# Performance work log

Hardware: AMD Instinct MI355X
Metric: run time of the kernel (lower is better)

Reference implementation:

```python
import jax, jax.numpy as jnp
import numpy as np

S, B, NINP, NHID, NLAYERS = 512, 128, 128, 128, 3


def setup_inputs() -> dict:
    key = jax.random.key(0)
    ks = jax.random.split(key, 6)
    stdv = 1.0 / float(np.sqrt(NHID))
    u = lambda k, shape: jax.random.uniform(k, shape, jnp.float32, -stdv, stdv)
    return {
        "x": jax.random.normal(ks[0], (S, B, NINP), jnp.float32),
        "lin_w": u(ks[1], (NHID, NINP)),
        "lin_b": u(ks[2], (NHID,)),
        "W": u(ks[3], (NLAYERS, 4 * NHID, NHID)),
        "U": u(ks[4], (NLAYERS, 4 * NHID, NLAYERS * NHID)),
        "G": u(ks[5], (NLAYERS, NHID, 1)),
    }


def reference(x, lin_w, lin_b, W, U, G):
    # x: [S, B, ninp]; eval mode (no dropout masks), feedback=True, gated=True.
    S_, B_, _ = x.shape
    L = W.shape[0]
    H = W.shape[1] // 4
    xp = x @ lin_w.T + lin_b  # [S, B, H] input projection
    h0 = jnp.zeros((L, B_, H), x.dtype)
    c0 = jnp.zeros((L, B_, H), x.dtype)

    def step(carry, xt):
        h, c = carry  # each [L, B, H]
        # gated: per-layer scalar sigmoid gate, broadcast over H
        gh = jax.nn.sigmoid(jnp.einsum('lbh,lho->lbo', h, G))  # [L, B, 1]
        h = gh * h
        # feedback: concat all layers' hidden along features, shared by every layer
        hx = h.transpose(1, 0, 2).reshape(B_, L * H)  # [B, L*H]
        inp = xt  # [B, H]; stacked layers: output of layer i feeds layer i+1
        hs, cs = [], []
        for i in range(L):
            gates = inp @ W[i].T + hx @ U[i].T  # [B, 4H]
            ig, fg, gg, og = jnp.split(gates, 4, axis=-1)
            ig = jax.nn.sigmoid(ig)
            fg = jax.nn.sigmoid(fg)
            gg = jnp.tanh(gg)
            og = jax.nn.sigmoid(og)
            cy = fg * c[i] + ig * gg
            hy = og * jnp.tanh(cy)
            hs.append(hy)
            cs.append(cy)
            inp = hy
        return (jnp.stack(hs, 0), jnp.stack(cs, 0)), None

    (h, c), _ = jax.lax.scan(step, (h0, c0), xp)
    return (h, c)
```

## Files before the change

### kernel.cpp

```cpp
#include <hip/hip_runtime.h>

#define S_LEN 512
#define BATCH 128
#define NH    128
#define NL    3

#define HXS  392
#define INPS 136

#define XP_OFF   0u
#define WP_OFF   16777216u
#define UP_OFF   (WP_OFF + 393216u)
#define HX_OFF   (UP_OFF + 1179648u)
#define HX_SZ    393216u

typedef float f32x4 __attribute__((ext_vector_type(4)));
typedef short bf16x8 __attribute__((ext_vector_type(8)));
typedef unsigned u32x4 __attribute__((ext_vector_type(4)));
typedef unsigned long long u64;

__device__ __forceinline__ short f2bf(float f) {
    unsigned u = __builtin_bit_cast(unsigned, f);
    u = (u + 0x7FFFu + ((u >> 16) & 1u)) >> 16;
    return (short)u;
}
__device__ __forceinline__ float bf2f_lo(unsigned u) { return __builtin_bit_cast(float, u << 16); }
__device__ __forceinline__ float bf2f_hi(unsigned u) { return __builtin_bit_cast(float, u & 0xFFFF0000u); }
__device__ __forceinline__ float chf(const u32x4& q, int r) {
    unsigned wd = (r < 2) ? q[0] : q[1];
    return (r & 1) ? bf2f_hi(wd) : bf2f_lo(wd);
}
__device__ __forceinline__ float sigm(float x) { return 1.f / (1.f + __expf(-x)); }
__device__ __forceinline__ float tanh_fast(float x) { return 2.f / (1.f + __expf(-2.f * x)) - 1.f; }

__global__ __launch_bounds__(128) void xp_kernel(const float* __restrict__ x,
        const float* __restrict__ lin_w, const float* __restrict__ lin_b,
        short* __restrict__ xp) {
    __shared__ float xs[8 * 128];
    const int tid = threadIdx.x;
    const long r0 = (long)blockIdx.x * 8;
    for (int rr = 0; rr < 8; ++rr)
        xs[rr * 128 + tid] = x[(r0 + rr) * 128 + tid];
    __syncthreads();
    float acc[8];
    float bias = lin_b[tid];
    #pragma unroll
    for (int rr = 0; rr < 8; ++rr) acc[rr] = bias;
    const float* wrow = lin_w + (long)tid * 128;
    for (int k = 0; k < 128; ++k) {
        float wv = wrow[k];
        #pragma unroll
        for (int rr = 0; rr < 8; ++rr) acc[rr] += xs[rr * 128 + k] * wv;
    }
    for (int rr = 0; rr < 8; ++rr)
        xp[(r0 + rr) * 128 + tid] = f2bf(acc[rr]);
}

__global__ __launch_bounds__(256) void pack_kernel(const float* __restrict__ W,
        const float* __restrict__ U, short* __restrict__ Wp, short* __restrict__ Up) {
    int id = blockIdx.x * 256 + threadIdx.x;
    int lane = id & 63;
    int fid = id >> 6;
    int n = lane & 15, lk = lane >> 4;
    if (fid < 384) {
        int kt = fid & 3, w = (fid >> 2) & 3, unit = fid >> 4;
        int l = unit >> 3, c = unit & 7;
        int row = (n >> 2) * 128 + c * 16 + w * 4 + (n & 3);
        const float* src = W + ((long)(l * 512 + row)) * 128 + kt * 32 + lk * 8;
        short* dst = Wp + (long)fid * 512 + lane * 8;
        #pragma unroll
        for (int j = 0; j < 8; ++j) dst[j] = f2bf(src[j]);
    } else {
        int f = fid - 384;
        int kt = f % 12, gu = f / 12;
        int w = gu & 3, unit = gu >> 2;
        int l = unit >> 3, c = unit & 7;
        int row = (n >> 2) * 128 + c * 16 + w * 4 + (n & 3);
        const float* src = U + ((long)(l * 512 + row)) * 384 + kt * 32 + lk * 8;
        short* dst = Up + (long)f * 512 + lane * 8;
        #pragma unroll
        for (int j = 0; j < 8; ++j) dst[j] = f2bf(src[j]);
    }
}


__global__ __launch_bounds__(256, 1) void lstm_kernel(
    const short* __restrict__ xp, const short* __restrict__ Wp,
    const short* __restrict__ Up, const float* __restrict__ Gp,
    char* __restrict__ hexch, float* __restrict__ out)
{
    __shared__ short hx_lds[16 * HXS];
    __shared__ short inp_lds[16 * INPS];
    __shared__ float G_lds[NL * 128];
    __shared__ unsigned hxflag;

    const int tid  = threadIdx.x;
    const int lane = tid & 63;
    const int w    = tid >> 6;
    const int lr   = lane & 15;
    const int lk   = lane >> 4;
    const int grp  = blockIdx.x & 7;
    const int unit = blockIdx.x >> 3;
    const int l    = unit >> 3;
    const int c    = unit & 7;
    const int b0   = grp * 16;

    bf16x8 ufr[12], wfr[4];
    {
        const short* ub = Up + ((long)(unit * 4 + w) * 12) * 512 + lane * 8;
        #pragma unroll
        for (int kt = 0; kt < 12; ++kt) ufr[kt] = *(const bf16x8*)(ub + kt * 512);
        const short* wb = Wp + ((long)(unit * 4 + w) * 4) * 512 + lane * 8;
        #pragma unroll
        for (int kt = 0; kt < 4; ++kt) wfr[kt] = *(const bf16x8*)(wb + kt * 512);
    }
    #pragma unroll
    for (int kt = 0; kt < 12; ++kt) asm volatile("" : "+v"(ufr[kt]));
    #pragma unroll
    for (int kt = 0; kt < 4; ++kt)  asm volatile("" : "+v"(wfr[kt]));

    for (int i = tid; i < NL * 128; i += 256) G_lds[i] = Gp[i];
    for (int i = tid; i < 16 * HXS; i += 256) hx_lds[i] = 0;
    if (tid == 0) hxflag = 0;
    float c_reg[4] = {0.f, 0.f, 0.f, 0.f};
    __syncthreads();

    for (int t = 0; t < S_LEN; ++t) {
        const int par = t & 1;
        __syncthreads();

        bf16x8 xa[4];
        if (l == 0) {
            const short* xp_t = xp + ((long)t * BATCH + b0) * 128;
            #pragma unroll
            for (int kt = 0; kt < 4; ++kt)
                xa[kt] = *(const bf16x8*)(xp_t + lr * 128 + kt * 32 + lk * 8);
        }

        const int rg = lane >> 4, cg = lane & 15;
        if (t > 0 && w < 2) {
            const unsigned want = (unsigned)t;
            const u64 ab = (u64)(hexch + (size_t)((((par ^ 1) * 8 + grp) * 3 + w)) * 8192
                                       + (size_t)cg * 512 + (size_t)rg * 16);
            u32x4 q0, q1, q2, q3, q4, q5, q6, q7;
            for (int rounds = 0;; ++rounds) {
                asm volatile(
                    "global_load_dwordx4 %0, %8, off sc0 sc1\n\t"
                    "global_load_dwordx4 %1, %8, off offset:64 sc0 sc1\n\t"
                    "global_load_dwordx4 %2, %8, off offset:128 sc0 sc1\n\t"
                    "global_load_dwordx4 %3, %8, off offset:192 sc0 sc1\n\t"
                    "global_load_dwordx4 %4, %8, off offset:256 sc0 sc1\n\t"
                    "global_load_dwordx4 %5, %8, off offset:320 sc0 sc1\n\t"
                    "global_load_dwordx4 %6, %8, off offset:384 sc0 sc1\n\t"
                    "global_load_dwordx4 %7, %8, off offset:448 sc0 sc1\n\t"
                    "s_waitcnt vmcnt(0)"
                    : "=&v"(q0), "=&v"(q1), "=&v"(q2), "=&v"(q3),
                      "=&v"(q4), "=&v"(q5), "=&v"(q6), "=&v"(q7)
                    : "v"(ab) : "memory");
                bool fr = (q0[3] == want) && (q1[3] == want) && (q2[3] == want) && (q3[3] == want)
                       && (q4[3] == want) && (q5[3] == want) && (q6[3] == want) && (q7[3] == want);
                if (__all(fr) || rounds > 262144) break;
            }
            u32x4 qs[8] = {q0, q1, q2, q3, q4, q5, q6, q7};
            const float* gb = &G_lds[w * 128 + cg * 8];
            float s[4] = {0.f, 0.f, 0.f, 0.f};
            #pragma unroll
            for (int k = 0; k < 8; ++k) {
                float gk = gb[k];
                #pragma unroll
                for (int r = 0; r < 4; ++r) s[r] += chf(qs[k], r) * gk;
            }
            #pragma unroll
            for (int m = 1; m <= 8; m <<= 1)
                #pragma unroll
                for (int r = 0; r < 4; ++r) s[r] += __shfl_xor(s[r], m, 64);
            #pragma unroll
            for (int r = 0; r < 4; ++r) {
                float gh = sigm(s[r]);
                unsigned wd[4];
                #pragma unroll
                for (int jj = 0; jj < 4; ++jj)
                    wd[jj] = (unsigned)(unsigned short)f2bf(gh * chf(qs[2 * jj], r))
                           | ((unsigned)(unsigned short)f2bf(gh * chf(qs[2 * jj + 1], r)) << 16);
                *(u32x4*)&hx_lds[(rg * 4 + r) * HXS + w * 128 + cg * 8] =
                    (u32x4){wd[0], wd[1], wd[2], wd[3]};
            }
        }
        __syncthreads();

        if (t > 0 && w == 3) {
            const unsigned want = (unsigned)t;
            const u64 ab = (u64)(hexch + (size_t)((((par ^ 1) * 8 + grp) * 3 + 2)) * 8192
                                       + (size_t)cg * 512 + (size_t)rg * 16);
            u32x4 q0, q1, q2, q3, q4, q5, q6, q7;
            for (int rounds = 0;; ++rounds) {
                asm volatile(
                    "global_load_dwordx4 %0, %8, off sc0 sc1\n\t"
                    "global_load_dwordx4 %1, %8, off offset:64 sc0 sc1\n\t"
                    "global_load_dwordx4 %2, %8, off offset:128 sc0 sc1\n\t"
                    "global_load_dwordx4 %3, %8, off offset:192 sc0 sc1\n\t"
                    "global_load_dwordx4 %4, %8, off offset:256 sc0 sc1\n\t"
                    "global_load_dwordx4 %5, %8, off offset:320 sc0 sc1\n\t"
                    "global_load_dwordx4 %6, %8, off offset:384 sc0 sc1\n\t"
                    "global_load_dwordx4 %7, %8, off offset:448 sc0 sc1\n\t"
                    "s_waitcnt vmcnt(0)"
                    : "=&v"(q0), "=&v"(q1), "=&v"(q2), "=&v"(q3),
                      "=&v"(q4), "=&v"(q5), "=&v"(q6), "=&v"(q7)
                    : "v"(ab) : "memory");
                bool fr = (q0[3] == want) && (q1[3] == want) && (q2[3] == want) && (q3[3] == want)
                       && (q4[3] == want) && (q5[3] == want) && (q6[3] == want) && (q7[3] == want);
                if (__all(fr) || rounds > 262144) break;
            }
            u32x4 qs[8] = {q0, q1, q2, q3, q4, q5, q6, q7};
            const float* gb = &G_lds[2 * 128 + cg * 8];
            float s[4] = {0.f, 0.f, 0.f, 0.f};
            #pragma unroll
            for (int k = 0; k < 8; ++k) {
                float gk = gb[k];
                #pragma unroll
                for (int r = 0; r < 4; ++r) s[r] += chf(qs[k], r) * gk;
            }
            #pragma unroll
            for (int m = 1; m <= 8; m <<= 1)
                #pragma unroll
                for (int r = 0; r < 4; ++r) s[r] += __shfl_xor(s[r], m, 64);
            #pragma unroll
            for (int r = 0; r < 4; ++r) {
                float gh = sigm(s[r]);
                unsigned wd[4];
                #pragma unroll
                for (int jj = 0; jj < 4; ++jj)
                    wd[jj] = (unsigned)(unsigned short)f2bf(gh * chf(qs[2 * jj], r))
                           | ((unsigned)(unsigned short)f2bf(gh * chf(qs[2 * jj + 1], r)) << 16);
                *(u32x4*)&hx_lds[(rg * 4 + r) * HXS + 2 * 128 + cg * 8] =
                    (u32x4){wd[0], wd[1], wd[2], wd[3]};
            }
            if (lane == 0)
                __hip_atomic_store(&hxflag, (unsigned)t, __ATOMIC_RELEASE, __HIP_MEMORY_SCOPE_WORKGROUP);
        }

        f32x4 acc0 = (f32x4){0.f, 0.f, 0.f, 0.f};
        f32x4 acc1 = (f32x4){0.f, 0.f, 0.f, 0.f};
        #pragma unroll
        for (int kt = 0; kt < 8; ++kt) {
            bf16x8 a = *(const bf16x8*)&hx_lds[lr * HXS + kt * 32 + lk * 8];
            if (kt & 1) acc1 = __builtin_amdgcn_mfma_f32_16x16x32_bf16(a, ufr[kt], acc1, 0, 0, 0);
            else        acc0 = __builtin_amdgcn_mfma_f32_16x16x32_bf16(a, ufr[kt], acc0, 0, 0, 0);
        }
        if (t > 0) {
            int guard = 0;
            while (__hip_atomic_load(&hxflag, __ATOMIC_ACQUIRE, __HIP_MEMORY_SCOPE_WORKGROUP)
                   < (unsigned)t) {
                if (++guard > 40000000) break;
            }
        }
        #pragma unroll
        for (int kt = 8; kt < 12; ++kt) {
            bf16x8 a = *(const bf16x8*)&hx_lds[lr * HXS + kt * 32 + lk * 8];
            if (kt & 1) acc1 = __builtin_amdgcn_mfma_f32_16x16x32_bf16(a, ufr[kt], acc1, 0, 0, 0);
            else        acc0 = __builtin_amdgcn_mfma_f32_16x16x32_bf16(a, ufr[kt], acc0, 0, 0, 0);
        }

        if (l == 0) {
            #pragma unroll
            for (int kt = 0; kt < 4; ++kt) {
                if (kt & 1) acc1 = __builtin_amdgcn_mfma_f32_16x16x32_bf16(xa[kt], wfr[kt], acc1, 0, 0, 0);
                else        acc0 = __builtin_amdgcn_mfma_f32_16x16x32_bf16(xa[kt], wfr[kt], acc0, 0, 0, 0);
            }
        } else {
            const unsigned want = (unsigned)(t + 1);
            const u64 base = (u64)(hexch + (size_t)(((par * 8 + grp) * 3 + (l - 1))) * 8192);
            const u64 a0 = base + (size_t)tid * 16;
            const u64 a1 = a0 + 4096;
            u32x4 q0, q1;
            for (int rounds = 0;; ++rounds) {
                asm volatile(
                    "global_load_dwordx4 %0, %2, off sc0 sc1\n\t"
                    "global_load_dwordx4 %1, %3, off sc0 sc1\n\t"
                    "s_waitcnt vmcnt(0)"
                    : "=&v"(q0), "=&v"(q1) : "v"(a0), "v"(a1) : "memory");
                if (__all((q0[3] == want) && (q1[3] == want)) || rounds > 262144) break;
            }
            {
                int col0 = tid >> 2, rg0 = tid & 3;
                inp_lds[(rg0 * 4 + 0) * INPS + col0] = (short)(q0[0] & 0xffff);
                inp_lds[(rg0 * 4 + 1) * INPS + col0] = (short)(q0[0] >> 16);
                inp_lds[(rg0 * 4 + 2) * INPS + col0] = (short)(q0[1] & 0xffff);
                inp_lds[(rg0 * 4 + 3) * INPS + col0] = (short)(q0[1] >> 16);
                int m1 = tid + 256, col1 = m1 >> 2, rg1 = m1 & 3;
                inp_lds[(rg1 * 4 + 0) * INPS + col1] = (short)(q1[0] & 0xffff);
                inp_lds[(rg1 * 4 + 1) * INPS + col1] = (short)(q1[0] >> 16);
                inp_lds[(rg1 * 4 + 2) * INPS + col1] = (short)(q1[1] & 0xffff);
                inp_lds[(rg1 * 4 + 3) * INPS + col1] = (short)(q1[1] >> 16);
            }
            __syncthreads();
            #pragma unroll
            for (int kt = 0; kt < 4; ++kt) {
                bf16x8 a = *(const bf16x8*)&inp_lds[lr * INPS + kt * 32 + lk * 8];
                if (kt & 1) acc1 = __builtin_amdgcn_mfma_f32_16x16x32_bf16(a, wfr[kt], acc1, 0, 0, 0);
                else        acc0 = __builtin_amdgcn_mfma_f32_16x16x32_bf16(a, wfr[kt], acc0, 0, 0, 0);
            }
        }

        f32x4 ac = acc0 + acc1;
        f32x4 vf, vg, vo;
        #pragma unroll
        for (int r = 0; r < 4; ++r) {
            vf[r] = __shfl_xor(ac[r], 4, 64);
            vg[r] = __shfl_xor(ac[r], 8, 64);
            vo[r] = __shfl_xor(ac[r], 12, 64);
        }
        if (lr < 4) {
            unsigned hw[2];
            float hys[4], cns[4];
            #pragma unroll
            for (int r = 0; r < 4; ++r) {
                float ig = sigm(ac[r]);
                float fg = sigm(vf[r]);
                float gg = tanh_fast(vg[r]);
                float og = sigm(vo[r]);
                float cn = fg * c_reg[r] + ig * gg;
                c_reg[r] = cn;
                cns[r] = cn;
                hys[r] = og * tanh_fast(cn);
            }
            hw[0] = (unsigned)(unsigned short)f2bf(hys[0])
                  | ((unsigned)(unsigned short)f2bf(hys[1]) << 16);
            hw[1] = (unsigned)(unsigned short)f2bf(hys[2])
                  | ((unsigned)(unsigned short)f2bf(hys[3]) << 16);
            u32x4 dq = (u32x4){hw[0], hw[1], 0u, (unsigned)(t + 1)};
            const int col = c * 16 + w * 4 + lr;
            u64 pa = (u64)(hexch + (size_t)(((par * 8 + grp) * 3 + l)) * 8192
                                 + ((size_t)col * 4 + lk) * 16);
            asm volatile("global_store_dwordx4 %0, %1, off sc0 sc1" :: "v"(pa), "v"(dq) : "memory");
            if (t == S_LEN - 1) {
                #pragma unroll
                for (int r = 0; r < 4; ++r) {
                    long o = ((long)(l * BATCH + b0 + lk * 4 + r)) * NH + col;
                    out[o] = hys[r];
                    out[(long)NL * BATCH * NH + o] = cns[r];
                }
            }
        }
    }
}

extern "C" void kernel_launch(void* const* d_in, const int* in_sizes, int n_in,
                              void* d_out, int out_size, void* d_ws, size_t ws_size,
                              hipStream_t stream) {
    const float* x     = (const float*)d_in[0];
    const float* lin_w = (const float*)d_in[1];
    const float* lin_b = (const float*)d_in[2];
    const float* W     = (const float*)d_in[3];
    const float* U     = (const float*)d_in[4];
    const float* G     = (const float*)d_in[5];
    float* out = (float*)d_out;

    short* xp    = (short*)((char*)d_ws + XP_OFF);
    short* Wp    = (short*)((char*)d_ws + WP_OFF);
    short* Up    = (short*)((char*)d_ws + UP_OFF);
    char*  hexch = (char*)d_ws + HX_OFF;

    (void)hipMemsetAsync(hexch, 0, HX_SZ, stream);
    hipLaunchKernelGGL(xp_kernel,   dim3(8192), dim3(128), 0, stream, x, lin_w, lin_b, xp);
    hipLaunchKernelGGL(pack_kernel, dim3(384),  dim3(256), 0, stream, W, U, Wp, Up);
    hipLaunchKernelGGL(lstm_kernel, dim3(192),  dim3(256), 0, stream,
                       xp, Wp, Up, G, hexch, out);
}
```

Before: 3.295 ms.

## Publish row-major hidden copy so next layer loads MFMA fragments directly

Each block now writes its new hidden state twice into a doubled exchange buffer: the original column-major layout, plus a row-major copy laid out so the next layer's input tile can be loaded straight into MFMA A-fragments. This removes the LDS staging of the layer input, its transposing scatter, and an extra __syncthreads per step. The recurrent U-matrix MFMAs are also moved ahead of the wait on the third hidden layer, so that wait overlaps with matrix work. The cost is twice the global store traffic per step, extra cross-lane shuffles, and eight polled loads per lane instead of two.

```diff
diff --git a/kernel.cpp b/kernel.cpp
--- a/kernel.cpp
+++ b/kernel.cpp
@@ -6,13 +6,12 @@
 #define NL    3
 
 #define HXS  392
-#define INPS 136
 
 #define XP_OFF   0u
 #define WP_OFF   16777216u
 #define UP_OFF   (WP_OFF + 393216u)
 #define HX_OFF   (UP_OFF + 1179648u)
-#define HX_SZ    393216u
+#define HX_SZ    786432u
 
 typedef float f32x4 __attribute__((ext_vector_type(4)));
 typedef short bf16x8 __attribute__((ext_vector_type(8)));
@@ -90,7 +89,6 @@
     char* __restrict__ hexch, float* __restrict__ out)
 {
     __shared__ short hx_lds[16 * HXS];
-    __shared__ short inp_lds[16 * INPS];
     __shared__ float G_lds[NL * 128];
     __shared__ unsigned hxflag;
 
@@ -140,7 +138,7 @@
         const int rg = lane >> 4, cg = lane & 15;
         if (t > 0 && w < 2) {
             const unsigned want = (unsigned)t;
-            const u64 ab = (u64)(hexch + (size_t)((((par ^ 1) * 8 + grp) * 3 + w)) * 8192
+            const u64 ab = (u64)(hexch + (size_t)((((par ^ 1) * 8 + grp) * 3 + w)) * 16384
                                        + (size_t)cg * 512 + (size_t)rg * 16);
             u32x4 q0, q1, q2, q3, q4, q5, q6, q7;
             for (int rounds = 0;; ++rounds) {
@@ -188,9 +186,18 @@
         }
         __syncthreads();
 
+        f32x4 acc0 = (f32x4){0.f, 0.f, 0.f, 0.f};
+        f32x4 acc1 = (f32x4){0.f, 0.f, 0.f, 0.f};
+        #pragma unroll
+        for (int kt = 0; kt < 8; ++kt) {
+            bf16x8 a = *(const bf16x8*)&hx_lds[lr * HXS + kt * 32 + lk * 8];
+            if (kt & 1) acc1 = __builtin_amdgcn_mfma_f32_16x16x32_bf16(a, ufr[kt], acc1, 0, 0, 0);
+            else        acc0 = __builtin_amdgcn_mfma_f32_16x16x32_bf16(a, ufr[kt], acc0, 0, 0, 0);
+        }
+
         if (t > 0 && w == 3) {
             const unsigned want = (unsigned)t;
-            const u64 ab = (u64)(hexch + (size_t)((((par ^ 1) * 8 + grp) * 3 + 2)) * 8192
+            const u64 ab = (u64)(hexch + (size_t)((((par ^ 1) * 8 + grp) * 3 + 2)) * 16384
                                        + (size_t)cg * 512 + (size_t)rg * 16);
             u32x4 q0, q1, q2, q3, q4, q5, q6, q7;
             for (int rounds = 0;; ++rounds) {
@@ -238,15 +245,6 @@
             if (lane == 0)
                 __hip_atomic_store(&hxflag, (unsigned)t, __ATOMIC_RELEASE, __HIP_MEMORY_SCOPE_WORKGROUP);
         }
-
-        f32x4 acc0 = (f32x4){0.f, 0.f, 0.f, 0.f};
-        f32x4 acc1 = (f32x4){0.f, 0.f, 0.f, 0.f};
-        #pragma unroll
-        for (int kt = 0; kt < 8; ++kt) {
-            bf16x8 a = *(const bf16x8*)&hx_lds[lr * HXS + kt * 32 + lk * 8];
-            if (kt & 1) acc1 = __builtin_amdgcn_mfma_f32_16x16x32_bf16(a, ufr[kt], acc1, 0, 0, 0);
-            else        acc0 = __builtin_amdgcn_mfma_f32_16x16x32_bf16(a, ufr[kt], acc0, 0, 0, 0);
-        }
         if (t > 0) {
             int guard = 0;
             while (__hip_atomic_load(&hxflag, __ATOMIC_ACQUIRE, __HIP_MEMORY_SCOPE_WORKGROUP)
@@ -269,37 +267,36 @@
             }
         } else {
             const unsigned want = (unsigned)(t + 1);
-            const u64 base = (u64)(hexch + (size_t)(((par * 8 + grp) * 3 + (l - 1))) * 8192);
-            const u64 a0 = base + (size_t)tid * 16;
-            const u64 a1 = a0 + 4096;
-            u32x4 q0, q1;
+            const u64 rb = (u64)(hexch + (size_t)(((par * 8 + grp) * 3 + (l - 1))) * 16384 + 8192
+                                       + (size_t)lr * 512 + (size_t)lk * 32);
+            u32x4 p0, p1, p2, p3, p4, p5, p6, p7;
             for (int rounds = 0;; ++rounds) {
                 asm volatile(
-                    "global_load_dwordx4 %0, %2, off sc0 sc1\n\t"
-                    "global_load_dwordx4 %1, %3, off sc0 sc1\n\t"
+                    "global_load_dwordx4 %0, %8, off sc0 sc1\n\t"
+                    "global_load_dwordx4 %1, %8, off offset:16 sc0 sc1\n\t"
+                    "global_load_dwordx4 %2, %8, off offset:128 sc0 sc1\n\t"
+                    "global_load_dwordx4 %3, %8, off offset:144 sc0 sc1\n\t"
+                    "global_load_dwordx4 %4, %8, off offset:256 sc0 sc1\n\t"
+                    "global_load_dwordx4 %5, %8, off offset:272 sc0 sc1\n\t"
+                    "global_load_dwordx4 %6, %8, off offset:384 sc0 sc1\n\t"
+                    "global_load_dwordx4 %7, %8, off offset:400 sc0 sc1\n\t"
                     "s_waitcnt vmcnt(0)"
-                    : "=&v"(q0), "=&v"(q1) : "v"(a0), "v"(a1) : "memory");
-                if (__all((q0[3] == want) && (q1[3] == want)) || rounds > 262144) break;
-            }
-            {
-                int col0 = tid >> 2, rg0 = tid & 3;
-                inp_lds[(rg0 * 4 + 0) * INPS + col0] = (short)(q0[0] & 0xffff);
-                inp_lds[(rg0 * 4 + 1) * INPS + col0] = (short)(q0[0] >> 16);
-                inp_lds[(rg0 * 4 + 2) * INPS + col0] = (short)(q0[1] & 0xffff);
-                inp_lds[(rg0 * 4 + 3) * INPS + col0] = (short)(q0[1] >> 16);
-                int m1 = tid + 256, col1 = m1 >> 2, rg1 = m1 & 3;
-                inp_lds[(rg1 * 4 + 0) * INPS + col1] = (short)(q1[0] & 0xffff);
-                inp_lds[(rg1 * 4 + 1) * INPS + col1] = (short)(q1[0] >> 16);
-                inp_lds[(rg1 * 4 + 2) * INPS + col1] = (short)(q1[1] & 0xffff);
-                inp_lds[(rg1 * 4 + 3) * INPS + col1] = (short)(q1[1] >> 16);
-            }
-            __syncthreads();
-            #pragma unroll
-            for (int kt = 0; kt < 4; ++kt) {
-                bf16x8 a = *(const bf16x8*)&inp_lds[lr * INPS + kt * 32 + lk * 8];
-                if (kt & 1) acc1 = __builtin_amdgcn_mfma_f32_16x16x32_bf16(a, wfr[kt], acc1, 0, 0, 0);
-                else        acc0 = __builtin_amdgcn_mfma_f32_16x16x32_bf16(a, wfr[kt], acc0, 0, 0, 0);
-            }
+                    : "=&v"(p0), "=&v"(p1), "=&v"(p2), "=&v"(p3),
+                      "=&v"(p4), "=&v"(p5), "=&v"(p6), "=&v"(p7)
+                    : "v"(rb) : "memory");
+                bool fr = (p0[3] == want) && (p1[3] == want) && (p2[3] == want) && (p3[3] == want)
+                       && (p4[3] == want) && (p5[3] == want) && (p6[3] == want) && (p7[3] == want);
+                if (__all(fr) || rounds > 262144) break;
+            }
+            typedef unsigned u32x4v;
+            u32x4 fr0 = (u32x4){p0[0], p0[1], p1[0], p1[1]};
+            u32x4 fr1 = (u32x4){p2[0], p2[1], p3[0], p3[1]};
+            u32x4 fr2 = (u32x4){p4[0], p4[1], p5[0], p5[1]};
+            u32x4 fr3 = (u32x4){p6[0], p6[1], p7[0], p7[1]};
+            acc0 = __builtin_amdgcn_mfma_f32_16x16x32_bf16(__builtin_bit_cast(bf16x8, fr0), wfr[0], acc0, 0, 0, 0);
+            acc1 = __builtin_amdgcn_mfma_f32_16x16x32_bf16(__builtin_bit_cast(bf16x8, fr1), wfr[1], acc1, 0, 0, 0);
+            acc0 = __builtin_amdgcn_mfma_f32_16x16x32_bf16(__builtin_bit_cast(bf16x8, fr2), wfr[2], acc0, 0, 0, 0);
+            acc1 = __builtin_amdgcn_mfma_f32_16x16x32_bf16(__builtin_bit_cast(bf16x8, fr3), wfr[3], acc1, 0, 0, 0);
         }
 
         f32x4 ac = acc0 + acc1;
@@ -310,30 +307,57 @@
             vg[r] = __shfl_xor(ac[r], 8, 64);
             vo[r] = __shfl_xor(ac[r], 12, 64);
         }
-        if (lr < 4) {
-            unsigned hw[2];
+        {
+            unsigned hw0 = 0, hw1 = 0;
             float hys[4], cns[4];
-            #pragma unroll
-            for (int r = 0; r < 4; ++r) {
-                float ig = sigm(ac[r]);
-                float fg = sigm(vf[r]);
-                float gg = tanh_fast(vg[r]);
-                float og = sigm(vo[r]);
-                float cn = fg * c_reg[r] + ig * gg;
-                c_reg[r] = cn;
-                cns[r] = cn;
-                hys[r] = og * tanh_fast(cn);
-            }
-            hw[0] = (unsigned)(unsigned short)f2bf(hys[0])
-                  | ((unsigned)(unsigned short)f2bf(hys[1]) << 16);
-            hw[1] = (unsigned)(unsigned short)f2bf(hys[2])
-                  | ((unsigned)(unsigned short)f2bf(hys[3]) << 16);
-            u32x4 dq = (u32x4){hw[0], hw[1], 0u, (unsigned)(t + 1)};
-            const int col = c * 16 + w * 4 + lr;
-            u64 pa = (u64)(hexch + (size_t)(((par * 8 + grp) * 3 + l)) * 8192
-                                 + ((size_t)col * 4 + lk) * 16);
-            asm volatile("global_store_dwordx4 %0, %1, off sc0 sc1" :: "v"(pa), "v"(dq) : "memory");
-            if (t == S_LEN - 1) {
+            if (lr < 4) {
+                #pragma unroll
+                for (int r = 0; r < 4; ++r) {
+                    float ig = sigm(ac[r]);
+                    float fg = sigm(vf[r]);
+                    float gg = tanh_fast(vg[r]);
+                    float og = sigm(vo[r]);
+                    float cn = fg * c_reg[r] + ig * gg;
+                    c_reg[r] = cn;
+                    cns[r] = cn;
+                    hys[r] = og * tanh_fast(cn);
+                }
+                hw0 = (unsigned)(unsigned short)f2bf(hys[0])
+                    | ((unsigned)(unsigned short)f2bf(hys[1]) << 16);
+                hw1 = (unsigned)(unsigned short)f2bf(hys[2])
+                    | ((unsigned)(unsigned short)f2bf(hys[3]) << 16);
+            }
+            const u64 blk = (u64)(hexch + (size_t)(((par * 8 + grp) * 3 + l)) * 16384);
+            if (lr < 4) {
+                u32x4 dq = (u32x4){hw0, hw1, 0u, (unsigned)(t + 1)};
+                const int col = c * 16 + w * 4 + lr;
+                u64 pa = blk + ((size_t)col * 4 + lk) * 16;
+                asm volatile("global_store_dwordx4 %0, %1, off sc0 sc1" :: "v"(pa), "v"(dq) : "memory");
+            }
+            {
+                const int qb = (lane & ~3);
+                unsigned w00 = __shfl(hw0, qb + 0, 64), w01 = __shfl(hw0, qb + 1, 64);
+                unsigned w02 = __shfl(hw0, qb + 2, 64), w03 = __shfl(hw0, qb + 3, 64);
+                unsigned w10 = __shfl(hw1, qb + 0, 64), w11 = __shfl(hw1, qb + 1, 64);
+                unsigned w12 = __shfl(hw1, qb + 2, 64), w13 = __shfl(hw1, qb + 3, 64);
+                if (lr < 4) {
+                    unsigned s0 = (lr & 2) ? w10 : w00;
+                    unsigned s1 = (lr & 2) ? w11 : w01;
+                    unsigned s2 = (lr & 2) ? w12 : w02;
+                    unsigned s3 = (lr & 2) ? w13 : w03;
+                    unsigned e0 = (lr & 1) ? (s0 >> 16) : (s0 & 0xffffu);
+                    unsigned e1 = (lr & 1) ? (s1 >> 16) : (s1 & 0xffffu);
+                    unsigned e2 = (lr & 1) ? (s2 >> 16) : (s2 & 0xffffu);
+                    unsigned e3 = (lr & 1) ? (s3 >> 16) : (s3 & 0xffffu);
+                    u32x4 rq = (u32x4){e0 | (e1 << 16), e2 | (e3 << 16), 0u, (unsigned)(t + 1)};
+                    const int row = lk * 4 + lr;
+                    const int c4  = c * 4 + w;
+                    u64 ra = blk + 8192 + ((size_t)row * 32 + c4) * 16;
+                    asm volatile("global_store_dwordx4 %0, %1, off sc0 sc1" :: "v"(ra), "v"(rq) : "memory");
+                }
+            }
+            if (lr < 4 && t == S_LEN - 1) {
+                const int col = c * 16 + w * 4 + lr;
                 #pragma unroll
                 for (int r = 0; r < 4; ++r) {
                     long o = ((long)(l * BATCH + b0 + lk * 4 + r)) * NH + col;
```

Result: slower. 5.721 ms (+73.6%).
